# Kernel optimization log

Measured on AMD Instinct MI355X. Metric: run time of the kernel, lower is better.

## Reference

```python
import jax, jax.numpy as jnp
import numpy as np

B, DIM, H, W = 4, 384, 128, 128
HEADS = 8
EPS = 1e-12  # torch F.normalize eps


def setup_inputs() -> dict:
    key = jax.random.key(0)
    k0, k1, k2, k3 = jax.random.split(key, 4)
    x = jax.random.normal(k0, (B, DIM, H, W), jnp.float32)
    # 1x1 conv weights stored as [out, in] (kernel dims squeezed), no bias
    w_qkv = jax.random.normal(k1, (3 * DIM, DIM), jnp.float32) * 0.05
    # depthwise 3x3 conv, groups = 3*DIM -> weight [3*DIM, 1, 3, 3]
    w_dw = jax.random.normal(k2, (3 * DIM, 1, 3, 3), jnp.float32) * 0.05
    w_proj = jax.random.normal(k3, (DIM, DIM), jnp.float32) * 0.05
    temperature = jnp.ones((HEADS, 1, 1), jnp.float32)
    return {"x": x, "w_qkv": w_qkv, "w_dw": w_dw, "w_proj": w_proj,
            "temperature": temperature}


def reference(x, w_qkv, w_dw, w_proj, temperature):
    b, c, h, w = x.shape
    heads = temperature.shape[0]
    ch = c // heads  # per-head channel dim (softmax axis)

    # 1x1 conv (pointwise) == channel GEMM
    qkv = jnp.einsum('bchw,oc->bohw', x, w_qkv)  # [b, 3c, h, w]
    # depthwise 3x3 conv, padding=1
    qkv = jax.lax.conv_general_dilated(
        qkv, w_dw, window_strides=(1, 1), padding='SAME',
        feature_group_count=qkv.shape[1],
        dimension_numbers=('NCHW', 'OIHW', 'NCHW'))

    q, k, v = jnp.split(qkv, 3, axis=1)  # each [b, c, h, w]

    def to_heads(t):
        # b (head ch) h w -> b head ch (h w)
        return t.reshape(b, heads, ch, h * w)

    q, k, v = to_heads(q), to_heads(k), to_heads(v)

    # L2 normalize along spatial (last) axis, torch-style eps clamp
    q = q / jnp.maximum(jnp.linalg.norm(q, axis=-1, keepdims=True), EPS)
    k = k / jnp.maximum(jnp.linalg.norm(k, axis=-1, keepdims=True), EPS)

    # channel-wise (transposed) attention: [b, head, ch, ch]
    attn = jnp.einsum('bhcn,bhdn->bhcd', q, k) * temperature
    attn = jax.nn.softmax(attn, axis=-1)
    out = jnp.einsum('bhcd,bhdn->bhcn', attn, v)  # [b, head, ch, hw]

    out = out.reshape(b, c, h, w)
    return jnp.einsum('bchw,oc->bohw', out, w_proj)
```

## Files before the change

kernel.cpp:

```cpp
#include <hip/hip_runtime.h>
#include <math.h>

typedef unsigned short u16;
typedef unsigned int u32;
typedef __attribute__((ext_vector_type(8))) short bf16x8;
typedef __attribute__((ext_vector_type(4))) float f32x4;

#define IMG 128
#define HWN 16384
#define NTOT 65536
#define DIMC 384
#define CDIM 1152
#define NBATCH 4
#define NHEAD 8
#define CHD 48
#define KC 16
#define VSTR 152

__device__ __forceinline__ u16 f2bf(float f) {
  union { float f; u32 u; } x; x.f = f;
  u32 r = x.u + 0x7fffu + ((x.u >> 16) & 1u);
  return (u16)(r >> 16);
}
__device__ __forceinline__ float bf2f(u16 v) {
  union { u32 u; float f; } x; x.u = ((u32)v) << 16;
  return x.f;
}
__device__ __forceinline__ void gload_lds16(const u16* g, u16* lds) {
  __builtin_amdgcn_global_load_lds((const __attribute__((address_space(1))) void*)g,
                                   (__attribute__((address_space(3))) void*)lds, 16, 0, 0);
}

__global__ void convert_wq_kernel(const float* __restrict__ in, u16* __restrict__ out, int n) {
  int i = blockIdx.x * 256 + threadIdx.x;
  if (i < n) out[i] = f2bf(in[i]);
}

__global__ __launch_bounds__(256) void transpose_x_kernel(const float* __restrict__ x,
                                                          u16* __restrict__ xT) {
  __shared__ float tile[32][33];
  int n0 = blockIdx.x * 32, c0 = blockIdx.y * 32, b = blockIdx.z;
  const float* xb = x + (size_t)b * DIMC * HWN;
  u16* xTb = xT + (size_t)b * HWN * DIMC;
  int tx = threadIdx.x & 31, ty = threadIdx.x >> 5;
#pragma unroll
  for (int i = 0; i < 32; i += 8)
    tile[ty + i][tx] = xb[(size_t)(c0 + ty + i) * HWN + n0 + tx];
  __syncthreads();
  int cp = threadIdx.x & 15, nl = threadIdx.x >> 4;
#pragma unroll
  for (int i = 0; i < 2; i++) {
    int n = nl + i * 16;
    u32 o = (u32)f2bf(tile[cp * 2][n]) | ((u32)f2bf(tile[cp * 2 + 1][n]) << 16);
    *(u32*)&xTb[(size_t)(n0 + n) * DIMC + c0 + cp * 2] = o;
  }
}

template <int BF16OUT>
__global__ __launch_bounds__(256) void gemm_bt_kernel(
    const u16* __restrict__ A, const u16* __restrict__ B, void* __restrict__ Cout,
    int MBLK, int K, int lda, int ldb, int ldc,
    unsigned long long aStride, unsigned long long bStride, unsigned long long cStride) {
  __shared__ u16 As[128 * 64];
  __shared__ u16 Bs[128 * 64];
  int bz = blockIdx.z;
  const u16* Ab = A + (size_t)bz * aStride;
  const u16* Bb = B + (size_t)bz * bStride;
  int bid = blockIdx.x;
  int xcd = bid & 7, j = bid >> 3;
  int mb = j % MBLK, nb = (j / MBLK) * 8 + xcd;
  int n0 = nb * 128, m0 = mb * 128;
  int t = threadIdx.x;
  int wave = t >> 6, lane = t & 63;
  int wm = (wave >> 1) * 64, wn = (wave & 1) * 64;
  int lr = lane & 15;
  int g4 = lane >> 4;
  int lrow = lane >> 3;
  int lswz = ((lane & 7) ^ lrow) * 8;

  f32x4 acc[4][4];
#pragma unroll
  for (int mi = 0; mi < 4; mi++)
#pragma unroll
    for (int ni = 0; ni < 4; ni++) acc[mi][ni] = (f32x4){0.f, 0.f, 0.f, 0.f};

  for (int k0 = 0; k0 < K; k0 += 64) {
#pragma unroll
    for (int i = 0; i < 4; i++) {
      int r = wave * 32 + i * 8;
      gload_lds16(Ab + (size_t)(m0 + r + lrow) * lda + k0 + lswz, &As[r * 64]);
      gload_lds16(Bb + (size_t)(n0 + r + lrow) * ldb + k0 + lswz, &Bs[r * 64]);
    }
    __syncthreads();
#pragma unroll
    for (int kk = 0; kk < 2; kk++) {
      bf16x8 af[4], bfr[4];
#pragma unroll
      for (int mi = 0; mi < 4; mi++) {
        int arow = wm + mi * 16 + lr;
        int aoct = (kk * 4 + g4) ^ (lr & 7);
        af[mi] = *(const bf16x8*)&As[arow * 64 + aoct * 8];
      }
#pragma unroll
      for (int ni = 0; ni < 4; ni++) {
        int brow = wn + ni * 16 + lr;
        int boct = (kk * 4 + g4) ^ (lr & 7);
        bfr[ni] = *(const bf16x8*)&Bs[brow * 64 + boct * 8];
      }
#pragma unroll
      for (int mi = 0; mi < 4; mi++)
#pragma unroll
        for (int ni = 0; ni < 4; ni++)
          acc[mi][ni] = __builtin_amdgcn_mfma_f32_16x16x32_bf16(af[mi], bfr[ni],
                                                                acc[mi][ni], 0, 0, 0);
    }
    __syncthreads();
  }
  int r0 = (lane >> 4) * 4;
#pragma unroll
  for (int mi = 0; mi < 4; mi++)
#pragma unroll
    for (int ni = 0; ni < 4; ni++)
#pragma unroll
      for (int r = 0; r < 4; r++) {
        int row = m0 + wm + mi * 16 + r0 + r;
        int col = n0 + wn + ni * 16 + (lane & 15);
        size_t idx = (size_t)bz * cStride + (size_t)row * ldc + col;
        if (BF16OUT)
          ((u16*)Cout)[idx] = f2bf(acc[mi][ni][r]);
        else
          ((float*)Cout)[idx] = acc[mi][ni][r];
      }
}

__global__ __launch_bounds__(256) void dwconv_planar_kernel(const u16* __restrict__ qkvP,
                                                            const float* __restrict__ w_dw,
                                                            u16* __restrict__ qkvCP,
                                                            float* __restrict__ nrmp) {
  __shared__ u16 lrows[18 * 144];
  __shared__ float red[4];
  int strip = blockIdx.x, ch = blockIdx.y, b = blockIdx.z;
  int ys = strip * 16;
  int t = threadIdx.x;
  const u16* plane = qkvP + (size_t)ch * NTOT + b * HWN;
  u16* oplane = qkvCP + (size_t)ch * NTOT + b * HWN;

#pragma unroll
  for (int it = 0; it < 2; it++) {
    int ul = t + it * 256;
    if (ul < 324) {
      int row = ul / 18, u = ul % 18;
      int gy = ys - 1 + row;
      bf16x8 v = {0, 0, 0, 0, 0, 0, 0, 0};
      if (u >= 1 && u <= 16 && gy >= 0 && gy < 128)
        v = *(const bf16x8*)&plane[gy * IMG + (u - 1) * 8];
      *(bf16x8*)((char*)lrows + row * 288 + u * 16) = v;
    }
  }
  float wt[9];
#pragma unroll
  for (int r = 0; r < 9; r++) wt[r] = w_dw[ch * 9 + r];
  __syncthreads();

  int xo = t & 15, yl = t >> 4;
  float win[3][10];
#pragma unroll
  for (int d = 0; d < 3; d++) {
    const char* base = (const char*)lrows + (yl + d) * 288 + xo * 16;
    bf16x8 rA = *(const bf16x8*)(base);
    bf16x8 rB = *(const bf16x8*)(base + 16);
    bf16x8 rC = *(const bf16x8*)(base + 32);
    win[d][0] = bf2f((u16)rA[7]);
#pragma unroll
    for (int k2 = 0; k2 < 8; k2++) win[d][k2 + 1] = bf2f((u16)rB[k2]);
    win[d][9] = bf2f((u16)rC[0]);
  }
  float accv[8] = {0.f, 0.f, 0.f, 0.f, 0.f, 0.f, 0.f, 0.f};
#pragma unroll
  for (int d = 0; d < 3; d++)
#pragma unroll
    for (int dx = 0; dx < 3; dx++) {
      float w = wt[d * 3 + dx];
#pragma unroll
      for (int jj = 0; jj < 8; jj++) accv[jj] += win[d][jj + dx] * w;
    }
  bf16x8 o;
  float n2 = 0.f;
#pragma unroll
  for (int jj = 0; jj < 8; jj++) {
    o[jj] = (short)f2bf(accv[jj]);
    n2 += accv[jj] * accv[jj];
  }
  *(bf16x8*)&oplane[(ys + yl) * IMG + xo * 8] = o;

#pragma unroll
  for (int off2 = 32; off2 >= 1; off2 >>= 1) n2 += __shfl_xor(n2, off2);
  if ((t & 63) == 0) red[t >> 6] = n2;
  __syncthreads();
  if (t == 0)
    nrmp[((size_t)b * 8 + strip) * 768 + ch] = red[0] + red[1] + red[2] + red[3];
}

__global__ __launch_bounds__(256) void dwconv_vtrans_kernel(const u16* __restrict__ qkvP,
                                                            const float* __restrict__ w_dw,
                                                            u16* __restrict__ vT) {
  __shared__ u16 in3[3 * 32 * VSTR];
  __shared__ u16 ot[128 * 40];
  int y = blockIdx.x, cg = blockIdx.y, b = blockIdx.z;
  int t = threadIdx.x;
  int ch0 = 768 + cg * 32;

  if (t < 192) {
    int d = t / 64, r = t & 63;
    int ch = r >> 1, side = r & 1;
    *(bf16x8*)&in3[(d * 32 + ch) * VSTR + side * 136] = (bf16x8){0, 0, 0, 0, 0, 0, 0, 0};
  }
#pragma unroll
  for (int i = 0; i < 6; i++) {
    int u = t + i * 256;
    int d = u >> 9, ch = (u >> 4) & 31, o = u & 15;
    int yn = y - 1 + d;
    bf16x8 v = {0, 0, 0, 0, 0, 0, 0, 0};
    if (yn >= 0 && yn < 128)
      v = *(const bf16x8*)&qkvP[(size_t)(ch0 + ch) * NTOT + b * HWN + yn * IMG + o * 8];
    *(bf16x8*)&in3[(d * 32 + ch) * VSTR + 8 + o * 8] = v;
  }
  int c = t & 31;
  float wt[9];
#pragma unroll
  for (int r = 0; r < 9; r++) wt[r] = w_dw[(ch0 + c) * 9 + r];
  __syncthreads();

#pragma unroll
  for (int i = 0; i < 2; i++) {
    int oct = (t >> 5) + i * 8;
    float win[3][10];
#pragma unroll
    for (int d = 0; d < 3; d++) {
      const u16* base = &in3[(d * 32 + c) * VSTR + oct * 8];
      bf16x8 rA = *(const bf16x8*)(base);
      bf16x8 rB = *(const bf16x8*)(base + 8);
      bf16x8 rC = *(const bf16x8*)(base + 16);
      win[d][0] = bf2f((u16)rA[7]);
#pragma unroll
      for (int k2 = 0; k2 < 8; k2++) win[d][k2 + 1] = bf2f((u16)rB[k2]);
      win[d][9] = bf2f((u16)rC[0]);
    }
    float accv[8] = {0.f, 0.f, 0.f, 0.f, 0.f, 0.f, 0.f, 0.f};
#pragma unroll
    for (int d = 0; d < 3; d++)
#pragma unroll
      for (int dx = 0; dx < 3; dx++) {
        float w = wt[d * 3 + dx];
#pragma unroll
        for (int jj = 0; jj < 8; jj++) accv[jj] += win[d][jj + dx] * w;
      }
#pragma unroll
    for (int jj = 0; jj < 8; jj++) ot[(oct * 8 + jj) * 40 + c] = f2bf(accv[jj]);
  }
  __syncthreads();

#pragma unroll
  for (int i = 0; i < 2; i++) {
    int u = t + i * 256;
    int px = u >> 2, co = u & 3;
    bf16x8 v = *(const bf16x8*)&ot[px * 40 + co * 8];
    *(bf16x8*)&vT[((size_t)b * HWN + y * IMG + px) * DIMC + cg * 32 + co * 8] = v;
  }
}

__global__ __launch_bounds__(256) void gram_kernel(const u16* __restrict__ qkvCP,
                                                   float* __restrict__ partials) {
  __shared__ u16 qs[48 * 136];
  __shared__ u16 ks2[48 * 136];
  __shared__ float Sred[4 * 2304];
  int kc = blockIdx.x, h = blockIdx.y, b = blockIdx.z;
  int t = threadIdx.x, wave = t >> 6, lane = t & 63;
  int lr = lane & 15, lk = (lane >> 4) * 8;
  int nbase = b * HWN + kc * (HWN / KC);

  f32x4 acc[3][3];
#pragma unroll
  for (int mi = 0; mi < 3; mi++)
#pragma unroll
    for (int ni = 0; ni < 3; ni++) acc[mi][ni] = (f32x4){0.f, 0.f, 0.f, 0.f};

  for (int tile = 0; tile < (HWN / KC) / 128; tile++) {
    int n0 = nbase + tile * 128;
    __syncthreads();
#pragma unroll
    for (int i = 0; i < 6; i++) {
      int u = t + i * 256;
      int m = (u >= 768) ? 1 : 0;
      int uu = u - m * 768;
      int r = uu >> 4, cu = uu & 15;
      int chh = m ? 384 + h * CHD + r : h * CHD + r;
      bf16x8 v = *(const bf16x8*)&qkvCP[(size_t)chh * NTOT + n0 + cu * 8];
      *(bf16x8*)((char*)(m ? ks2 : qs) + r * 272 + cu * 16) = v;
    }
    __syncthreads();
    bf16x8 af[3], bfr[3];
#pragma unroll
    for (int mi = 0; mi < 3; mi++)
      af[mi] = *(const bf16x8*)((char*)qs + (mi * 16 + lr) * 272 + wave * 64 + lk * 2);
#pragma unroll
    for (int ni = 0; ni < 3; ni++)
      bfr[ni] = *(const bf16x8*)((char*)ks2 + (ni * 16 + lr) * 272 + wave * 64 + lk * 2);
#pragma unroll
    for (int mi = 0; mi < 3; mi++)
#pragma unroll
      for (int ni = 0; ni < 3; ni++)
        acc[mi][ni] = __builtin_amdgcn_mfma_f32_16x16x32_bf16(af[mi], bfr[ni],
                                                              acc[mi][ni], 0, 0, 0);
  }

#pragma unroll
  for (int mi = 0; mi < 3; mi++)
#pragma unroll
    for (int ni = 0; ni < 3; ni++)
#pragma unroll
      for (int r = 0; r < 4; r++) {
        int crow = mi * 16 + (lane >> 4) * 4 + r;
        int dcol = ni * 16 + (lane & 15);
        Sred[wave * 2304 + crow * 48 + dcol] = acc[mi][ni][r];
      }
  __syncthreads();
  float* pout = partials + ((size_t)((b * NHEAD + h) * KC + kc)) * 2304;
  for (int idx = t; idx < 2304; idx += 256) {
    float s = 0.f;
#pragma unroll
    for (int w = 0; w < 4; w++) s += Sred[w * 2304 + idx];
    pout[idx] = s;
  }
}

__global__ __launch_bounds__(256) void softmax_kernel(const float* __restrict__ partials,
                                                      const float* __restrict__ nrmp,
                                                      const float* __restrict__ temp,
                                                      float* __restrict__ attn) {
  __shared__ float S[2304];
  __shared__ float nq[48], nk[48];
  int h = blockIdx.x, b = blockIdx.y;
  const float* p = partials + (size_t)(b * NHEAD + h) * KC * 2304;
  for (int idx = threadIdx.x; idx < 2304; idx += 256) {
    float s = 0.f;
#pragma unroll
    for (int kc = 0; kc < KC; kc++) s += p[kc * 2304 + idx];
    S[idx] = s;
  }
  if (threadIdx.x < 96) {
    int tq = threadIdx.x;
    int c = (tq < 48) ? tq : tq - 48;
    int ch = (tq < 48) ? h * CHD + c : DIMC + h * CHD + c;
    float s = 0.f;
#pragma unroll
    for (int st = 0; st < 8; st++) s += nrmp[((size_t)b * 8 + st) * 768 + ch];
    float nv = fmaxf(sqrtf(s), 1e-12f);
    if (tq < 48) nq[c] = nv; else nk[c] = nv;
  }
  __syncthreads();
  float tf = temp[h];
  float* A = attn + (size_t)(b * NHEAD + h) * 2304;
  if (threadIdx.x < CHD) {
    int c = threadIdx.x;
    float inq = 1.f / nq[c];
    float mx = -1e30f;
    float row[48];
    for (int d = 0; d < CHD; d++) {
      float v = S[c * 48 + d] * tf * inq / nk[d];
      row[d] = v;
      mx = fmaxf(mx, v);
    }
    float sum = 0.f;
    for (int d = 0; d < CHD; d++) {
      float e = expf(row[d] - mx);
      row[d] = e;
      sum += e;
    }
    float inv = 1.f / sum;
    for (int d = 0; d < CHD; d++) A[c * 48 + d] = row[d] * inv;
  }
}

__global__ __launch_bounds__(256) void build_mf_kernel(const float* __restrict__ attn,
                                                       const float* __restrict__ w_proj,
                                                       u16* __restrict__ Mf) {
  __shared__ float al[NHEAD * 2304];
  int b = blockIdx.y, o0 = blockIdx.x * 32;
  for (int i = threadIdx.x; i < NHEAD * 2304; i += 256)
    al[i] = attn[(size_t)b * NHEAD * 2304 + i];
  __syncthreads();
  for (int idx = threadIdx.x; idx < 32 * DIMC; idx += 256) {
    int ol = idx / DIMC, cp = idx % DIMC;
    int o = o0 + ol, h = cp / CHD, d = cp % CHD;
    float s = 0.f;
#pragma unroll
    for (int c = 0; c < CHD; c++)
      s += w_proj[(size_t)o * DIMC + h * CHD + c] * al[h * 2304 + c * 48 + d];
    Mf[((size_t)b * DIMC + o) * DIMC + cp] = f2bf(s);
  }
}

extern "C" void kernel_launch(void* const* d_in, const int* in_sizes, int n_in,
                              void* d_out, int out_size, void* d_ws, size_t ws_size,
                              hipStream_t stream) {
  const float* x      = (const float*)d_in[0];
  const float* w_qkv  = (const float*)d_in[1];
  const float* w_dw   = (const float*)d_in[2];
  const float* w_proj = (const float*)d_in[3];
  const float* temp   = (const float*)d_in[4];
  float* out = (float*)d_out;

  char* ws = (char*)d_ws;
  size_t off = 0;
  u16* xT = (u16*)(ws + off);
  size_t xT_off = off;
  off += (size_t)NTOT * DIMC * 2;
  u16* qkvP = (u16*)(ws + off);
  off += (size_t)CDIM * NTOT * 2;
  u16* qkvCP = (u16*)(ws + off);
  off += (size_t)768 * NTOT * 2;
  u16* wq16 = (u16*)(ws + off);
  off += (size_t)CDIM * DIMC * 2;
  float* nrmp = (float*)(ws + off);
  off += (size_t)NBATCH * 8 * 768 * 4;
  float* partials = (float*)(ws + off);
  off += (size_t)NBATCH * NHEAD * KC * 2304 * 4;
  float* attn = (float*)(ws + off);
  off += (size_t)NBATCH * NHEAD * 2304 * 4;
  u16* Mf = (u16*)(ws + off);
  off += (size_t)NBATCH * DIMC * DIMC * 2;
  u16* vT = (u16*)(ws + xT_off);

  if (ws_size < off) return;

  convert_wq_kernel<<<dim3((CDIM * DIMC + 255) / 256), dim3(256), 0, stream>>>(
      w_qkv, wq16, CDIM * DIMC);
  transpose_x_kernel<<<dim3(HWN / 32, DIMC / 32, NBATCH), dim3(256), 0, stream>>>(x, xT);
  gemm_bt_kernel<1><<<dim3(4608, 1, 1), dim3(256), 0, stream>>>(
      wq16, xT, (void*)qkvP, 9, DIMC, DIMC, DIMC, NTOT, 0ULL, 0ULL, 0ULL);
  dwconv_planar_kernel<<<dim3(8, 768, NBATCH), dim3(256), 0, stream>>>(
      qkvP, w_dw, qkvCP, nrmp);
  dwconv_vtrans_kernel<<<dim3(IMG, 12, NBATCH), dim3(256), 0, stream>>>(qkvP, w_dw, vT);
  gram_kernel<<<dim3(KC, NHEAD, NBATCH), dim3(256), 0, stream>>>(qkvCP, partials);
  softmax_kernel<<<dim3(NHEAD, NBATCH), dim3(256), 0, stream>>>(partials, nrmp, temp, attn);
  build_mf_kernel<<<dim3(DIMC / 32, NBATCH), dim3(256), 0, stream>>>(attn, w_proj, Mf);
  gemm_bt_kernel<0><<<dim3(384, 1, NBATCH), dim3(256), 0, stream>>>(
      Mf, vT, (void*)out, 3, DIMC, DIMC, DIMC, HWN,
      (unsigned long long)DIMC * DIMC, (unsigned long long)HWN * DIMC,
      (unsigned long long)DIMC * HWN);
}
```

Before: 340.8 us.

## Replace QKV projection GEMM with 256x256-tile 8-phase pipelined kernel

Swaps the generic 128x128 bf16 GEMM for the 1x1 QKV conv with a dedicated 512-thread kernel using 256x256 tiles. It double-buffers K-slices in LDS through async global-to-LDS loads, interleaving them with MFMA phases under explicit vmcnt waits and barriers. The weight matrix is zero-padded from 1152 to 1280 rows so M divides into 256 tiles. This aims for more data reuse per tile and better overlap of loads with compute, at the cost of about 11% wasted rows of compute and writes, and a larger workspace.

```diff
diff --git a/kernel.cpp b/kernel.cpp
--- a/kernel.cpp
+++ b/kernel.cpp
@@ -11,6 +11,7 @@
 #define NTOT 65536
 #define DIMC 384
 #define CDIM 1152
+#define MPAD 1280
 #define NBATCH 4
 #define NHEAD 8
 #define CHD 48
@@ -30,10 +31,12 @@
   __builtin_amdgcn_global_load_lds((const __attribute__((address_space(1))) void*)g,
                                    (__attribute__((address_space(3))) void*)lds, 16, 0, 0);
 }
+#define BAR() do { asm volatile("" ::: "memory"); __builtin_amdgcn_s_barrier(); \
+                   asm volatile("" ::: "memory"); } while (0)
 
 __global__ void convert_wq_kernel(const float* __restrict__ in, u16* __restrict__ out, int n) {
   int i = blockIdx.x * 256 + threadIdx.x;
-  if (i < n) out[i] = f2bf(in[i]);
+  if (i < n) out[i] = (i < CDIM * DIMC) ? f2bf(in[i]) : (u16)0;
 }
 
 __global__ __launch_bounds__(256) void transpose_x_kernel(const float* __restrict__ x,
@@ -54,6 +57,112 @@
     u32 o = (u32)f2bf(tile[cp * 2][n]) | ((u32)f2bf(tile[cp * 2 + 1][n]) << 16);
     *(u32*)&xTb[(size_t)(n0 + n) * DIMC + c0 + cp * 2] = o;
   }
+}
+
+#define REG_OFF(op, par, h) (((op) * 4 + (par) * 2 + (h)) * 8192)
+
+__global__ __launch_bounds__(512, 2) void gemm1_8phase_kernel(
+    const u16* __restrict__ A, const u16* __restrict__ B, u16* __restrict__ C) {
+  __shared__ u16 lds[8 * 8192];
+  int bid = blockIdx.x;
+  int xcd = bid & 7, j = bid >> 3;
+  int mb = j % 5, nb = (j / 5) * 8 + xcd;
+  int m0 = mb * 256, n0 = nb * 256;
+  int t = threadIdx.x;
+  int wave = t >> 6, lane = t & 63;
+  int wm = wave >> 2, wn = wave & 3;
+  int lr = lane & 15, g4 = lane >> 4;
+  int srow = lane >> 3;
+  int soct = ((lane & 7) ^ srow) * 8;
+
+  auto STAGE = [&](int op, int par, int h, int ks) {
+    const u16* src = op ? B : A;
+    int rowbase = (op ? n0 : m0) + h * 128;
+    int kcol = ks * 64;
+#pragma unroll
+    for (int jj = 0; jj < 2; jj++) {
+      int blk = jj * 8 + wave;
+      gload_lds16(src + (size_t)(rowbase + blk * 8 + srow) * DIMC + kcol + soct,
+                  &lds[REG_OFF(op, par, h) + blk * 512]);
+    }
+  };
+
+  f32x4 acc[8][4];
+#pragma unroll
+  for (int mf = 0; mf < 8; mf++)
+#pragma unroll
+    for (int nf = 0; nf < 4; nf++) acc[mf][nf] = (f32x4){0.f, 0.f, 0.f, 0.f};
+
+  STAGE(1, 0, 0, 0); STAGE(1, 0, 1, 0);
+  STAGE(0, 0, 0, 0); STAGE(0, 0, 1, 0);
+  STAGE(1, 1, 0, 1); STAGE(1, 1, 1, 1);
+  asm volatile("s_waitcnt vmcnt(4)" ::: "memory");
+  BAR();
+
+  bf16x8 bfr[4][2];
+#pragma unroll
+  for (int iter = 0; iter < 3; ++iter) {
+#pragma unroll
+    for (int p = 0; p < 8; ++p) {
+      const int ks = p >> 2, q = p & 3;
+      if (q == 0) {
+#pragma unroll
+        for (int nf = 0; nf < 4; nf++)
+#pragma unroll
+          for (int kk = 0; kk < 2; kk++) {
+            int rowT = wn * 64 + nf * 16 + lr;
+            int h = rowT >> 7, R = rowT & 127;
+            int oct = (kk * 4 + g4) ^ (R & 7);
+            bfr[nf][kk] = *(const bf16x8*)&lds[REG_OFF(1, ks, h) + R * 64 + oct * 8];
+          }
+      }
+      bf16x8 af[2][2];
+#pragma unroll
+      for (int mm = 0; mm < 2; mm++)
+#pragma unroll
+        for (int kk = 0; kk < 2; kk++) {
+          int R = (q * 2 + mm) * 16 + lr;
+          int oct = (kk * 4 + g4) ^ (R & 7);
+          af[mm][kk] = *(const bf16x8*)&lds[REG_OFF(0, ks, wm) + R * 64 + oct * 8];
+        }
+      if (p == 0) STAGE(0, 1, 0, 2 * iter + 1);
+      if (p == 1) STAGE(0, 1, 1, 2 * iter + 1);
+      if (p == 2 && iter < 2) STAGE(1, 0, 0, 2 * iter + 2);
+      if (p == 3 && iter < 2) STAGE(1, 0, 1, 2 * iter + 2);
+      if (p == 4 && iter < 2) STAGE(0, 0, 0, 2 * iter + 2);
+      if (p == 5 && iter < 2) STAGE(0, 0, 1, 2 * iter + 2);
+      if (p == 6 && iter < 2) STAGE(1, 1, 0, 2 * iter + 3);
+      if (p == 7 && iter < 2) STAGE(1, 1, 1, 2 * iter + 3);
+      if (p == 3) {
+        if (iter == 2) asm volatile("s_waitcnt vmcnt(0)" ::: "memory");
+        else           asm volatile("s_waitcnt vmcnt(4)" ::: "memory");
+      }
+      if (p == 7 && iter < 2) asm volatile("s_waitcnt vmcnt(4)" ::: "memory");
+      BAR();
+      __builtin_amdgcn_s_setprio(1);
+#pragma unroll
+      for (int mm = 0; mm < 2; mm++)
+#pragma unroll
+        for (int nf = 0; nf < 4; nf++)
+#pragma unroll
+          for (int kk = 0; kk < 2; kk++)
+            acc[q * 2 + mm][nf] = __builtin_amdgcn_mfma_f32_16x16x32_bf16(
+                af[mm][kk], bfr[nf][kk], acc[q * 2 + mm][nf], 0, 0, 0);
+      __builtin_amdgcn_s_setprio(0);
+      BAR();
+    }
+  }
+
+#pragma unroll
+  for (int mf = 0; mf < 8; mf++)
+#pragma unroll
+    for (int nf = 0; nf < 4; nf++)
+#pragma unroll
+      for (int r = 0; r < 4; r++) {
+        int row = m0 + wm * 128 + mf * 16 + g4 * 4 + r;
+        int col = n0 + wn * 64 + nf * 16 + lr;
+        C[(size_t)row * NTOT + col] = f2bf(acc[mf][nf][r]);
+      }
 }
 
 template <int BF16OUT>
@@ -417,11 +526,11 @@
   size_t xT_off = off;
   off += (size_t)NTOT * DIMC * 2;
   u16* qkvP = (u16*)(ws + off);
-  off += (size_t)CDIM * NTOT * 2;
+  off += (size_t)MPAD * NTOT * 2;
   u16* qkvCP = (u16*)(ws + off);
   off += (size_t)768 * NTOT * 2;
   u16* wq16 = (u16*)(ws + off);
-  off += (size_t)CDIM * DIMC * 2;
+  off += (size_t)MPAD * DIMC * 2;
   float* nrmp = (float*)(ws + off);
   off += (size_t)NBATCH * 8 * 768 * 4;
   float* partials = (float*)(ws + off);
@@ -434,11 +543,10 @@
 
   if (ws_size < off) return;
 
-  convert_wq_kernel<<<dim3((CDIM * DIMC + 255) / 256), dim3(256), 0, stream>>>(
-      w_qkv, wq16, CDIM * DIMC);
+  convert_wq_kernel<<<dim3((MPAD * DIMC + 255) / 256), dim3(256), 0, stream>>>(
+      w_qkv, wq16, MPAD * DIMC);
   transpose_x_kernel<<<dim3(HWN / 32, DIMC / 32, NBATCH), dim3(256), 0, stream>>>(x, xT);
-  gemm_bt_kernel<1><<<dim3(4608, 1, 1), dim3(256), 0, stream>>>(
-      wq16, xT, (void*)qkvP, 9, DIMC, DIMC, DIMC, NTOT, 0ULL, 0ULL, 0ULL);
+  gemm1_8phase_kernel<<<dim3(1280, 1, 1), dim3(512), 0, stream>>>(wq16, xT, qkvP);
   dwconv_planar_kernel<<<dim3(8, 768, NBATCH), dim3(256), 0, stream>>>(
       qkvP, w_dw, qkvCP, nrmp);
   dwconv_vtrans_kernel<<<dim3(IMG, 12, NBATCH), dim3(256), 0, stream>>>(qkvP, w_dw, vT);
```

Result: no change. 345.5 us (+1.4%).
